# Kernel optimization log

Hardware: AMD Instinct MI355X
Metric: run time of the kernel (lower is better)

## Reference

```python
import jax, jax.numpy as jnp
import numpy as np

D_MODEL = 1024
NHEAD = 16
HEAD_DIM = D_MODEL // NHEAD


def setup_inputs() -> dict:
    key = jax.random.key(0)
    ks = jax.random.split(key, 11)
    B, S = 2, 2048
    s = 1.0 / np.sqrt(D_MODEL)
    return {
        "query": jax.random.normal(ks[0], (B, S, D_MODEL), jnp.float32),
        "key": jax.random.normal(ks[1], (B, S, D_MODEL), jnp.float32),
        "value": jax.random.normal(ks[2], (B, S, D_MODEL), jnp.float32),
        "wq_w": jax.random.normal(ks[3], (D_MODEL, D_MODEL), jnp.float32) * s,
        "wq_b": jax.random.normal(ks[4], (D_MODEL,), jnp.float32) * s,
        "wk_w": jax.random.normal(ks[5], (D_MODEL, D_MODEL), jnp.float32) * s,
        "wk_b": jax.random.normal(ks[6], (D_MODEL,), jnp.float32) * s,
        "wv_w": jax.random.normal(ks[7], (D_MODEL, D_MODEL), jnp.float32) * s,
        "wv_b": jax.random.normal(ks[8], (D_MODEL,), jnp.float32) * s,
        "wo_w": jax.random.normal(ks[9], (D_MODEL, D_MODEL), jnp.float32) * s,
        "wo_b": jax.random.normal(ks[10], (D_MODEL,), jnp.float32) * s,
    }


def reference(query, key, value, wq_w, wq_b, wk_w, wk_b, wv_w, wv_b, wo_w, wo_b):
    B, S, _ = query.shape
    # torch Linear: x @ W.T + b
    def proj(x, w, b):
        y = x @ w.T + b
        return y.reshape(B, S, NHEAD, HEAD_DIM).transpose(0, 2, 1, 3)  # [B,H,S,Dh]

    Q = proj(query, wq_w, wq_b)
    K = proj(key, wk_w, wk_b)
    V = proj(value, wv_w, wv_b)

    scale = 1.0 / np.sqrt(HEAD_DIM).astype(np.float32)
    scores = jnp.einsum("bhqd,bhkd->bhqk", Q, K) * scale  # [B,H,S,S]
    causal = jnp.tril(jnp.ones((S, S), dtype=bool))
    scores = jnp.where(causal, scores, -jnp.inf)
    attn = jax.nn.softmax(scores, axis=-1)
    out = jnp.einsum("bhqk,bhkd->bhqd", attn, V)  # [B,H,S,Dh]
    out = out.transpose(0, 2, 1, 3).reshape(B, S, D_MODEL)
    return out @ wo_w.T + wo_b
```

## Files before the change

### kernel.cpp

```cpp
#include <hip/hip_runtime.h>
#include <stdint.h>

#define D_MODEL 1024
#define S_LEN   2048
#define NHEAD   16
#define HEAD_DIM 64
#define BATCH   2
#define M_TOT   (BATCH * S_LEN)
#define Q_SCALE 0.18033688011112042f

using bf16x8 = __attribute__((ext_vector_type(8))) short;
using f32x4  = __attribute__((ext_vector_type(4))) float;

__device__ __forceinline__ unsigned short f2bf(float f) {
  union { float f; unsigned int u; } v; v.f = f;
  unsigned int u = v.u;
  return (unsigned short)((u + 0x7FFFu + ((u >> 16) & 1u)) >> 16);
}
__device__ __forceinline__ unsigned int pkbf(float a, float b) {
#if __has_builtin(__builtin_amdgcn_cvt_pk_bf16_f32)
  auto p = __builtin_amdgcn_cvt_pk_bf16_f32(a, b);
  union { decltype(p) v; unsigned int u; } c; c.v = p;
  return c.u;
#else
  return (unsigned int)f2bf(a) | ((unsigned int)f2bf(b) << 16);
#endif
}
__device__ __forceinline__ bf16x8 cvt8(const float* p) {
  const float4 a = *(const float4*)p;
  const float4 b = *(const float4*)(p + 4);
  union { unsigned int u[4]; bf16x8 v; } r;
  r.u[0] = pkbf(a.x, a.y); r.u[1] = pkbf(a.z, a.w);
  r.u[2] = pkbf(b.x, b.y); r.u[3] = pkbf(b.z, b.w);
  return r.v;
}
__device__ __forceinline__ float fexp2(float x) {
#if __has_builtin(__builtin_amdgcn_exp2f)
  return __builtin_amdgcn_exp2f(x);
#else
  return __expf(x * 0.69314718055994531f);
#endif
}
__device__ __forceinline__ void async16(const unsigned short* g, short* l) {
  __builtin_amdgcn_global_load_lds(
      reinterpret_cast<const __attribute__((address_space(1))) unsigned int*>(
          reinterpret_cast<uintptr_t>(g)),
      reinterpret_cast<__attribute__((address_space(3))) unsigned int*>(
          reinterpret_cast<uintptr_t>(l)),
      16, 0, 0);
}

#define LDK 40

__global__ __launch_bounds__(256)
void cast_all(const float* __restrict__ wq, const float* __restrict__ wk,
              const float* __restrict__ wv, const float* __restrict__ wo,
              const float* __restrict__ q, const float* __restrict__ k,
              const float* __restrict__ v,
              unsigned short* __restrict__ wb,
              unsigned short* __restrict__ qb, unsigned short* __restrict__ kb,
              unsigned short* __restrict__ vb)
{
  const int z = blockIdx.y;
  const float* src;
  unsigned short* d;
  size_t n;
  switch (z) {
    case 0: src = wq; d = wb;                                   n = (size_t)D_MODEL * D_MODEL; break;
    case 1: src = wk; d = wb + (size_t)1 * D_MODEL * D_MODEL;   n = (size_t)D_MODEL * D_MODEL; break;
    case 2: src = wv; d = wb + (size_t)2 * D_MODEL * D_MODEL;   n = (size_t)D_MODEL * D_MODEL; break;
    case 3: src = wo; d = wb + (size_t)3 * D_MODEL * D_MODEL;   n = (size_t)D_MODEL * D_MODEL; break;
    case 4: src = q;  d = qb;                                   n = (size_t)M_TOT * D_MODEL;   break;
    case 5: src = k;  d = kb;                                   n = (size_t)M_TOT * D_MODEL;   break;
    default: src = v; d = vb;                                   n = (size_t)M_TOT * D_MODEL;   break;
  }
  const size_t i = ((size_t)blockIdx.x * 256 + threadIdx.x) * 8;
  if (i < n) *(bf16x8*)(d + i) = cvt8(src + i);
}

__device__ __forceinline__ void gemm_tile_lds(const unsigned short* __restrict__ A,
                                              const unsigned short* __restrict__ W,
                                              int m0, int n0,
                                              short* As, short* Bs,
                                              f32x4 acc[4][4])
{
  const int t    = threadIdx.x;
  const int lane = t & 63;
  const int w    = t >> 6;
  const int quad = lane >> 4;
  const int l16  = lane & 15;
  const int wm   = (w >> 1) * 64;
  const int wn   = (w & 1) * 64;
  const int srow = w * 16 + (lane >> 2);
  const int scol = (lane & 3) * 8;

  for (int mt = 0; mt < 4; ++mt)
    for (int nt = 0; nt < 4; ++nt)
      acc[mt][nt] = f32x4{0.f, 0.f, 0.f, 0.f};

  for (int kt = 0; kt < D_MODEL / 32; ++kt) {
    const int kc = kt * 32 + scol;
    __syncthreads();
    async16(A + (size_t)(m0 + srow)      * D_MODEL + kc, As + srow * 32 + scol);
    async16(A + (size_t)(m0 + 64 + srow) * D_MODEL + kc, As + (64 + srow) * 32 + scol);
    async16(W + (size_t)(n0 + srow)      * D_MODEL + kc, Bs + srow * 32 + scol);
    async16(W + (size_t)(n0 + 64 + srow) * D_MODEL + kc, Bs + (64 + srow) * 32 + scol);
    __syncthreads();

    bf16x8 af[4], bfr[4];
    for (int mt = 0; mt < 4; ++mt)
      af[mt] = *(const bf16x8*)(As + (wm + mt * 16 + l16) * 32 + quad * 8);
    for (int nt = 0; nt < 4; ++nt)
      bfr[nt] = *(const bf16x8*)(Bs + (wn + nt * 16 + l16) * 32 + quad * 8);
    for (int mt = 0; mt < 4; ++mt)
      for (int nt = 0; nt < 4; ++nt)
        acc[mt][nt] = __builtin_amdgcn_mfma_f32_16x16x32_bf16(af[mt], bfr[nt], acc[mt][nt], 0, 0, 0);
  }
}

__device__ __forceinline__ void gemm_tile_f32(const float* __restrict__ A,
                                              const unsigned short* __restrict__ W,
                                              int m0, int n0,
                                              short* As, short* Bs,
                                              f32x4 acc[4][4])
{
  const int t    = threadIdx.x;
  const int lane = t & 63;
  const int w    = t >> 6;
  const int quad = lane >> 4;
  const int l16  = lane & 15;
  const int wm   = (w >> 1) * 64;
  const int wn   = (w & 1) * 64;
  const int srow = t >> 2;
  const int scol = (t & 3) * 8;

  for (int mt = 0; mt < 4; ++mt)
    for (int nt = 0; nt < 4; ++nt)
      acc[mt][nt] = f32x4{0.f, 0.f, 0.f, 0.f};

  for (int kt = 0; kt < D_MODEL / 32; ++kt) {
    const int kc = kt * 32 + scol;
    const bf16x8 a0 = cvt8(A + (size_t)(m0 + srow)      * D_MODEL + kc);
    const bf16x8 a1 = cvt8(A + (size_t)(m0 + srow + 64) * D_MODEL + kc);
    const bf16x8 b0 = *(const bf16x8*)(W + (size_t)(n0 + srow)      * D_MODEL + kc);
    const bf16x8 b1 = *(const bf16x8*)(W + (size_t)(n0 + srow + 64) * D_MODEL + kc);
    __syncthreads();
    *(bf16x8*)(As + (srow)      * LDK + scol) = a0;
    *(bf16x8*)(As + (srow + 64) * LDK + scol) = a1;
    *(bf16x8*)(Bs + (srow)      * LDK + scol) = b0;
    *(bf16x8*)(Bs + (srow + 64) * LDK + scol) = b1;
    __syncthreads();

    bf16x8 af[4], bfr[4];
    for (int mt = 0; mt < 4; ++mt)
      af[mt] = *(const bf16x8*)(As + (wm + mt * 16 + l16) * LDK + quad * 8);
    for (int nt = 0; nt < 4; ++nt)
      bfr[nt] = *(const bf16x8*)(Bs + (wn + nt * 16 + l16) * LDK + quad * 8);
    for (int mt = 0; mt < 4; ++mt)
      for (int nt = 0; nt < 4; ++nt)
        acc[mt][nt] = __builtin_amdgcn_mfma_f32_16x16x32_bf16(af[mt], bfr[nt], acc[mt][nt], 0, 0, 0);
  }
}

__device__ __forceinline__ void qkv_epilogue(int z, int m0, int n0,
                                             const float* __restrict__ bias,
                                             float scale,
                                             unsigned short* __restrict__ dst,
                                             f32x4 acc[4][4])
{
  const int t    = threadIdx.x;
  const int lane = t & 63;
  const int w    = t >> 6;
  const int quad = lane >> 4;
  const int l16  = lane & 15;
  const int wm   = (w >> 1) * 64;
  const int wn   = (w & 1) * 64;

  for (int nt = 0; nt < 4; ++nt) {
    const int n = n0 + wn + nt * 16 + l16;
    const float bb = bias[n];
    const int h = n >> 6, d = n & 63;
    for (int mt = 0; mt < 4; ++mt) {
      for (int r = 0; r < 4; ++r) {
        const int m = m0 + wm + mt * 16 + quad * 4 + r;
        const int b = m >> 11, s = m & 2047;
        const unsigned short val = f2bf((acc[mt][nt][r] + bb) * scale);
        if (z < 2)
          dst[((size_t)((b * NHEAD + h) * S_LEN + s)) * HEAD_DIM + d] = val;
        else
          dst[((size_t)((b * NHEAD + h) * HEAD_DIM + d)) * S_LEN + s] = val;
      }
    }
  }
}

__global__ __launch_bounds__(256)
void qkv_fast(const unsigned short* __restrict__ qb,
              const unsigned short* __restrict__ kb,
              const unsigned short* __restrict__ vb,
              const unsigned short* __restrict__ wqb,
              const unsigned short* __restrict__ wkb,
              const unsigned short* __restrict__ wvb,
              const float* __restrict__ bq, const float* __restrict__ bk,
              const float* __restrict__ bv,
              unsigned short* __restrict__ Qh, unsigned short* __restrict__ Kh,
              unsigned short* __restrict__ VhT)
{
  __shared__ __attribute__((aligned(16))) short As[128 * 32];
  __shared__ __attribute__((aligned(16))) short Bs[128 * 32];
  const int z = blockIdx.z;
  const unsigned short* A    = (z == 0) ? qb  : (z == 1) ? kb  : vb;
  const unsigned short* W    = (z == 0) ? wqb : (z == 1) ? wkb : wvb;
  const float*          bias = (z == 0) ? bq  : (z == 1) ? bk  : bv;
  unsigned short*       dst  = (z == 0) ? Qh  : (z == 1) ? Kh  : VhT;
  const float           scale = (z == 0) ? Q_SCALE : 1.0f;

  const int m0 = blockIdx.x * 128, n0 = blockIdx.y * 128;
  f32x4 acc[4][4];
  gemm_tile_lds(A, W, m0, n0, As, Bs, acc);
  qkv_epilogue(z, m0, n0, bias, scale, dst, acc);
}

__global__ __launch_bounds__(256)
void qkv_slow(const float* __restrict__ query, const float* __restrict__ key,
              const float* __restrict__ value,
              const unsigned short* __restrict__ wqb,
              const unsigned short* __restrict__ wkb,
              const unsigned short* __restrict__ wvb,
              const float* __restrict__ bq, const float* __restrict__ bk,
              const float* __restrict__ bv,
              unsigned short* __restrict__ Qh, unsigned short* __restrict__ Kh,
              unsigned short* __restrict__ VhT)
{
  __shared__ __attribute__((aligned(16))) short As[128 * LDK];
  __shared__ __attribute__((aligned(16))) short Bs[128 * LDK];
  const int z = blockIdx.z;
  const float*          A    = (z == 0) ? query : (z == 1) ? key : value;
  const unsigned short* W    = (z == 0) ? wqb   : (z == 1) ? wkb : wvb;
  const float*          bias = (z == 0) ? bq    : (z == 1) ? bk  : bv;
  unsigned short*       dst  = (z == 0) ? Qh    : (z == 1) ? Kh  : VhT;
  const float           scale = (z == 0) ? Q_SCALE : 1.0f;

  const int m0 = blockIdx.x * 128, n0 = blockIdx.y * 128;
  f32x4 acc[4][4];
  gemm_tile_f32(A, W, m0, n0, As, Bs, acc);
  qkv_epilogue(z, m0, n0, bias, scale, dst, acc);
}

__global__ __launch_bounds__(256)
void out_proj(const unsigned short* __restrict__ Oh,
              const unsigned short* __restrict__ wob,
              const float* __restrict__ bo,
              float* __restrict__ dst)
{
  __shared__ __attribute__((aligned(16))) short As[128 * 32];
  __shared__ __attribute__((aligned(16))) short Bs[128 * 32];
  const int m0 = blockIdx.x * 128, n0 = blockIdx.y * 128;
  f32x4 acc[4][4];
  gemm_tile_lds(Oh, wob, m0, n0, As, Bs, acc);

  const int t    = threadIdx.x;
  const int lane = t & 63;
  const int w    = t >> 6;
  const int quad = lane >> 4;
  const int l16  = lane & 15;
  const int wm   = (w >> 1) * 64;
  const int wn   = (w & 1) * 64;

  for (int nt = 0; nt < 4; ++nt) {
    const int n = n0 + wn + nt * 16 + l16;
    const float bb = bo[n];
    for (int mt = 0; mt < 4; ++mt)
      for (int r = 0; r < 4; ++r) {
        const int m = m0 + wm + mt * 16 + quad * 4 + r;
        dst[(size_t)m * D_MODEL + n] = acc[mt][nt][r] + bb;
      }
  }
}

__global__ __launch_bounds__(256)
void attn_kernel(const unsigned short* __restrict__ Qh,
                 const unsigned short* __restrict__ Kh,
                 const unsigned short* __restrict__ VhT,
                 unsigned short* __restrict__ O)
{
  __shared__ __attribute__((aligned(16))) short Ks[128 * 72];
  __shared__ __attribute__((aligned(16))) short Vts[64 * 136];
  __shared__ __attribute__((aligned(16))) short Ps[4][16 * 136];

  const int bh   = blockIdx.x;
  const int qt   = (int)gridDim.y - 1 - (int)blockIdx.y;
  const int q0   = qt * 64;
  const int b    = bh >> 4;
  const int h    = bh & 15;
  const int t    = threadIdx.x;
  const int w    = t >> 6;
  const int lane = t & 63;
  const int quad = lane >> 4;
  const int l16  = lane & 15;
  const size_t headK = (size_t)bh * S_LEN * HEAD_DIM;
  const size_t headV = (size_t)bh * HEAD_DIM * S_LEN;

  bf16x8 qf[2];
  {
    const size_t qrow = (size_t)bh * S_LEN + (q0 + w * 16 + l16);
    qf[0] = *(const bf16x8*)(Qh + qrow * HEAD_DIM + quad * 8);
    qf[1] = *(const bf16x8*)(Qh + qrow * HEAD_DIM + 32 + quad * 8);
  }
  bf16x8 ones;
  for (int j = 0; j < 8; ++j) ones[j] = (short)0x3F80;

  f32x4 lacc = f32x4{0.f, 0.f, 0.f, 0.f};
  f32x4 oacc[4];
  for (int dt = 0; dt < 4; ++dt) oacc[dt] = f32x4{0.f, 0.f, 0.f, 0.f};

  const int rowbase = q0 + w * 16;
  const int rowmax  = rowbase + 15;
  const int kr = t >> 3, kc = (t & 7) * 8;
  const int vd = t >> 4, vc = (t & 15) * 8;

  const int nkt = (qt + 2) >> 1;
  for (int kt = 0; kt < nkt; ++kt) {
    const int k0 = kt * 128;
    __syncthreads();
    for (int i = 0; i < 4; ++i) {
      const int rr = kr + i * 32;
      *(bf16x8*)(Ks + rr * 72 + kc) =
          *(const bf16x8*)(Kh + headK + (size_t)(k0 + rr) * HEAD_DIM + kc);
      const int dd = vd + i * 16;
      *(bf16x8*)(Vts + dd * 136 + vc) =
          *(const bf16x8*)(VhT + headV + (size_t)dd * S_LEN + k0 + vc);
    }
    __syncthreads();

    float st[8][4];
    for (int nt = 0; nt < 8; ++nt) {
      const int c0 = k0 + nt * 16;
      if (c0 <= rowmax) {
        f32x4 s = f32x4{0.f, 0.f, 0.f, 0.f};
        for (int ks = 0; ks < 2; ++ks) {
          const bf16x8 kf = *(const bf16x8*)(Ks + (nt * 16 + l16) * 72 + ks * 32 + quad * 8);
          s = __builtin_amdgcn_mfma_f32_16x16x32_bf16(qf[ks], kf, s, 0, 0, 0);
        }
        if (c0 + 15 <= rowbase) {
          for (int r = 0; r < 4; ++r) st[nt][r] = fexp2(s[r]);
        } else {
          const int colg = c0 + l16;
          for (int r = 0; r < 4; ++r) {
            const int rowg = rowbase + quad * 4 + r;
            st[nt][r] = (colg <= rowg) ? fexp2(s[r]) : 0.f;
          }
        }
      } else {
        for (int r = 0; r < 4; ++r) st[nt][r] = 0.f;
      }
    }
    for (int nt = 0; nt < 8; nt += 2) {
      for (int r = 0; r < 4; ++r) {
        const unsigned int u = pkbf(st[nt][r], st[nt + 1][r]);
        short* base = &Ps[w][(quad * 4 + r) * 136 + nt * 16 + l16];
        base[0]  = (short)(u & 0xffffu);
        base[16] = (short)(u >> 16);
      }
    }

    for (int ks = 0; ks < 4; ++ks) {
      if (k0 + ks * 32 > rowmax) break;
      const bf16x8 pf = *(const bf16x8*)(&Ps[w][0] + l16 * 136 + ks * 32 + quad * 8);
      lacc = __builtin_amdgcn_mfma_f32_16x16x32_bf16(pf, ones, lacc, 0, 0, 0);
      for (int dt = 0; dt < 4; ++dt) {
        const bf16x8 vf = *(const bf16x8*)(Vts + (dt * 16 + l16) * 136 + ks * 32 + quad * 8);
        oacc[dt] = __builtin_amdgcn_mfma_f32_16x16x32_bf16(pf, vf, oacc[dt], 0, 0, 0);
      }
    }
  }

  for (int dt = 0; dt < 4; ++dt) {
    for (int r = 0; r < 4; ++r) {
      const int rowg = q0 + w * 16 + quad * 4 + r;
      O[(size_t)(b * S_LEN + rowg) * D_MODEL + h * 64 + dt * 16 + l16] =
          f2bf(oacc[dt][r] / lacc[r]);
    }
  }
}

extern "C" void kernel_launch(void* const* d_in, const int* in_sizes, int n_in,
                              void* d_out, int out_size, void* d_ws, size_t ws_size,
                              hipStream_t stream)
{
  (void)in_sizes; (void)n_in; (void)out_size;
  const float* q  = (const float*)d_in[0];
  const float* k  = (const float*)d_in[1];
  const float* v  = (const float*)d_in[2];
  const float* wq = (const float*)d_in[3];
  const float* bq = (const float*)d_in[4];
  const float* wk = (const float*)d_in[5];
  const float* bk = (const float*)d_in[6];
  const float* wv = (const float*)d_in[7];
  const float* bv = (const float*)d_in[8];
  const float* wo = (const float*)d_in[9];
  const float* bo = (const float*)d_in[10];
  float* out = (float*)d_out;

  unsigned short* wb  = (unsigned short*)d_ws;
  unsigned short* wqb = wb;
  unsigned short* wkb = wb + (size_t)1 * D_MODEL * D_MODEL;
  unsigned short* wvb = wb + (size_t)2 * D_MODEL * D_MODEL;
  unsigned short* wob = wb + (size_t)3 * D_MODEL * D_MODEL;
  unsigned short* Kh  = wb + (size_t)4 * D_MODEL * D_MODEL;
  unsigned short* VhT = Kh + (size_t)M_TOT * D_MODEL;
  unsigned short* Oh  = VhT + (size_t)M_TOT * D_MODEL;
  unsigned short* qb  = Oh;
  unsigned short* vb  = Oh + (size_t)M_TOT * D_MODEL;
  unsigned short* Qh  = (unsigned short*)d_out;
  unsigned short* kb  = Qh + (size_t)M_TOT * D_MODEL;

  const bool fast = ws_size >= (size_t)40 * 1024 * 1024;

  dim3 g1(M_TOT / 128, D_MODEL / 128, 3);
  if (fast) {
    dim3 gc((size_t)M_TOT * D_MODEL / (256 * 8), 7, 1);
    cast_all<<<gc, 256, 0, stream>>>(wq, wk, wv, wo, q, k, v, wb, qb, kb, vb);
    qkv_fast<<<g1, 256, 0, stream>>>(qb, kb, vb, wqb, wkb, wvb, bq, bk, bv, Qh, Kh, VhT);
  } else {
    dim3 gc((size_t)D_MODEL * D_MODEL / (256 * 8), 4, 1);
    cast_all<<<gc, 256, 0, stream>>>(wq, wk, wv, wo, q, k, v, wb, qb, kb, vb);
    qkv_slow<<<g1, 256, 0, stream>>>(q, k, v, wqb, wkb, wvb, bq, bk, bv, Qh, Kh, VhT);
  }

  dim3 g2(BATCH * NHEAD, S_LEN / 64, 1);
  attn_kernel<<<g2, 256, 0, stream>>>(Qh, Kh, VhT, Oh);

  dim3 g3(M_TOT / 128, D_MODEL / 128, 1);
  out_proj<<<g3, 256, 0, stream>>>(Oh, wob, bo, out);
}
```

Before: 224.5 us.

## Enlarge attention query tile to 128 rows per block, two row-tiles per warp

```diff
diff --git a/kernel.cpp b/kernel.cpp
--- a/kernel.cpp
+++ b/kernel.cpp
@@ -290,7 +290,7 @@
 
   const int bh   = blockIdx.x;
   const int qt   = (int)gridDim.y - 1 - (int)blockIdx.y;
-  const int q0   = qt * 64;
+  const int q0   = qt * 128;
   const int b    = bh >> 4;
   const int h    = bh & 15;
   const int t    = threadIdx.x;
@@ -301,25 +301,26 @@
   const size_t headK = (size_t)bh * S_LEN * HEAD_DIM;
   const size_t headV = (size_t)bh * HEAD_DIM * S_LEN;
 
-  bf16x8 qf[2];
-  {
-    const size_t qrow = (size_t)bh * S_LEN + (q0 + w * 16 + l16);
-    qf[0] = *(const bf16x8*)(Qh + qrow * HEAD_DIM + quad * 8);
-    qf[1] = *(const bf16x8*)(Qh + qrow * HEAD_DIM + 32 + quad * 8);
+  bf16x8 qf[2][2];
+  for (int m = 0; m < 2; ++m) {
+    const size_t qrow = (size_t)bh * S_LEN + (q0 + w * 32 + m * 16 + l16);
+    qf[m][0] = *(const bf16x8*)(Qh + qrow * HEAD_DIM + quad * 8);
+    qf[m][1] = *(const bf16x8*)(Qh + qrow * HEAD_DIM + 32 + quad * 8);
   }
   bf16x8 ones;
   for (int j = 0; j < 8; ++j) ones[j] = (short)0x3F80;
 
-  f32x4 lacc = f32x4{0.f, 0.f, 0.f, 0.f};
-  f32x4 oacc[4];
-  for (int dt = 0; dt < 4; ++dt) oacc[dt] = f32x4{0.f, 0.f, 0.f, 0.f};
-
-  const int rowbase = q0 + w * 16;
-  const int rowmax  = rowbase + 15;
+  f32x4 lacc[2];
+  f32x4 oacc[2][4];
+  for (int m = 0; m < 2; ++m) {
+    lacc[m] = f32x4{0.f, 0.f, 0.f, 0.f};
+    for (int dt = 0; dt < 4; ++dt) oacc[m][dt] = f32x4{0.f, 0.f, 0.f, 0.f};
+  }
+
   const int kr = t >> 3, kc = (t & 7) * 8;
   const int vd = t >> 4, vc = (t & 15) * 8;
 
-  const int nkt = (qt + 2) >> 1;
+  const int nkt = qt + 1;
   for (int kt = 0; kt < nkt; ++kt) {
     const int k0 = kt * 128;
     __syncthreads();
@@ -333,53 +334,61 @@
     }
     __syncthreads();
 
-    float st[8][4];
-    for (int nt = 0; nt < 8; ++nt) {
-      const int c0 = k0 + nt * 16;
-      if (c0 <= rowmax) {
-        f32x4 s = f32x4{0.f, 0.f, 0.f, 0.f};
-        for (int ks = 0; ks < 2; ++ks) {
-          const bf16x8 kf = *(const bf16x8*)(Ks + (nt * 16 + l16) * 72 + ks * 32 + quad * 8);
-          s = __builtin_amdgcn_mfma_f32_16x16x32_bf16(qf[ks], kf, s, 0, 0, 0);
+    for (int m = 0; m < 2; ++m) {
+      const int rowbase = q0 + w * 32 + m * 16;
+      const int rowmax  = rowbase + 15;
+      if (k0 > rowmax) continue;
+
+      float st[8][4];
+      for (int nt = 0; nt < 8; ++nt) {
+        const int c0 = k0 + nt * 16;
+        if (c0 <= rowmax) {
+          f32x4 s = f32x4{0.f, 0.f, 0.f, 0.f};
+          for (int ks = 0; ks < 2; ++ks) {
+            const bf16x8 kf = *(const bf16x8*)(Ks + (nt * 16 + l16) * 72 + ks * 32 + quad * 8);
+            s = __builtin_amdgcn_mfma_f32_16x16x32_bf16(qf[m][ks], kf, s, 0, 0, 0);
+          }
+          if (c0 + 15 <= rowbase) {
+            for (int r = 0; r < 4; ++r) st[nt][r] = fexp2(s[r]);
+          } else {
+            const int colg = c0 + l16;
+            for (int r = 0; r < 4; ++r) {
+              const int rowg = rowbase + quad * 4 + r;
+              st[nt][r] = (colg <= rowg) ? fexp2(s[r]) : 0.f;
+            }
+          }
+        } else {
+          for (int r = 0; r < 4; ++r) st[nt][r] = 0.f;
         }
-        if (c0 + 15 <= rowbase) {
-          for (int r = 0; r < 4; ++r) st[nt][r] = fexp2(s[r]);
-        } else {
-          const int colg = c0 + l16;
-          for (int r = 0; r < 4; ++r) {
-            const int rowg = rowbase + quad * 4 + r;
-            st[nt][r] = (colg <= rowg) ? fexp2(s[r]) : 0.f;
-          }
+      }
+      for (int nt = 0; nt < 8; nt += 2) {
+        for (int r = 0; r < 4; ++r) {
+          const unsigned int u = pkbf(st[nt][r], st[nt + 1][r]);
+          short* base = &Ps[w][(quad * 4 + r) * 136 + nt * 16 + l16];
+          base[0]  = (short)(u & 0xffffu);
+          base[16] = (short)(u >> 16);
         }
-      } else {
-        for (int r = 0; r < 4; ++r) st[nt][r] = 0.f;
+      }
+
+      for (int ks = 0; ks < 4; ++ks) {
+        if (k0 + ks * 32 > rowmax) break;
+        const bf16x8 pf = *(const bf16x8*)(&Ps[w][0] + l16 * 136 + ks * 32 + quad * 8);
+        lacc[m] = __builtin_amdgcn_mfma_f32_16x16x32_bf16(pf, ones, lacc[m], 0, 0, 0);
+        for (int dt = 0; dt < 4; ++dt) {
+          const bf16x8 vf = *(const bf16x8*)(Vts + (dt * 16 + l16) * 136 + ks * 32 + quad * 8);
+          oacc[m][dt] = __builtin_amdgcn_mfma_f32_16x16x32_bf16(pf, vf, oacc[m][dt], 0, 0, 0);
+        }
       }
     }
-    for (int nt = 0; nt < 8; nt += 2) {
+  }
+
+  for (int m = 0; m < 2; ++m) {
+    for (int dt = 0; dt < 4; ++dt) {
       for (int r = 0; r < 4; ++r) {
-        const unsigned int u = pkbf(st[nt][r], st[nt + 1][r]);
-        short* base = &Ps[w][(quad * 4 + r) * 136 + nt * 16 + l16];
-        base[0]  = (short)(u & 0xffffu);
-        base[16] = (short)(u >> 16);
-      }
-    }
-
-    for (int ks = 0; ks < 4; ++ks) {
-      if (k0 + ks * 32 > rowmax) break;
-      const bf16x8 pf = *(const bf16x8*)(&Ps[w][0] + l16 * 136 + ks * 32 + quad * 8);
-      lacc = __builtin_amdgcn_mfma_f32_16x16x32_bf16(pf, ones, lacc, 0, 0, 0);
-      for (int dt = 0; dt < 4; ++dt) {
-        const bf16x8 vf = *(const bf16x8*)(Vts + (dt * 16 + l16) * 136 + ks * 32 + quad * 8);
-        oacc[dt] = __builtin_amdgcn_mfma_f32_16x16x32_bf16(pf, vf, oacc[dt], 0, 0, 0);
-      }
-    }
-  }
-
-  for (int dt = 0; dt < 4; ++dt) {
-    for (int r = 0; r < 4; ++r) {
-      const int rowg = q0 + w * 16 + quad * 4 + r;
-      O[(size_t)(b * S_LEN + rowg) * D_MODEL + h * 64 + dt * 16 + l16] =
-          f2bf(oacc[dt][r] / lacc[r]);
+        const int rowg = q0 + w * 32 + m * 16 + quad * 4 + r;
+        O[(size_t)(b * S_LEN + rowg) * D_MODEL + h * 64 + dt * 16 + l16] =
+            f2bf(oacc[m][dt][r] / lacc[m][r]);
+      }
     }
   }
 }
@@ -428,7 +437,7 @@
     qkv_slow<<<g1, 256, 0, stream>>>(q, k, v, wqb, wkb, wvb, bq, bk, bv, Qh, Kh, VhT);
   }
 
-  dim3 g2(BATCH * NHEAD, S_LEN / 64, 1);
+  dim3 g2(BATCH * NHEAD, S_LEN / 128, 1);
   attn_kernel<<<g2, 256, 0, stream>>>(Qh, Kh, VhT, Oh);
 
   dim3 g3(M_TOT / 128, D_MODEL / 128, 1);
```

Result: slower. 245.9 us (+9.5%).
